# Optimization experiments

Measured on AMD Instinct MI355X. Metric: run time of the kernel, lower is better.

## Reference

```python
import jax, jax.numpy as jnp
import numpy as np

EMBED_DIM = 1024
N_HEADS = 16

def setup_inputs() -> dict:
    key = jax.random.key(0)
    ks = jax.random.split(key, 5)
    C = EMBED_DIM
    std = 1.0 / np.sqrt(C)
    x = jax.random.normal(ks[0], (2, 2048, C), dtype=jnp.float32)
    w_attn = jax.random.normal(ks[1], (C, 3 * C), dtype=jnp.float32) * std  # (in, out)
    b_attn = jax.random.normal(ks[2], (3 * C,), dtype=jnp.float32) * 0.01
    w_proj = jax.random.normal(ks[3], (C, C), dtype=jnp.float32) * std
    b_proj = jax.random.normal(ks[4], (C,), dtype=jnp.float32) * 0.01
    return {"x": x, "w_attn": w_attn, "b_attn": b_attn, "w_proj": w_proj, "b_proj": b_proj}

def reference(x, w_attn, b_attn, w_proj, b_proj):
    B, T, C = x.shape
    H = N_HEADS
    D = C // H
    qkv = x @ w_attn + b_attn                      # (B, T, 3C)
    q, k, v = jnp.split(qkv, 3, axis=2)
    # (B, T, C) -> (B, H, T, D)
    q = q.reshape(B, T, H, D).transpose(0, 2, 1, 3)
    k = k.reshape(B, T, H, D).transpose(0, 2, 1, 3)
    v = v.reshape(B, T, H, D).transpose(0, 2, 1, 3)
    # Faithful to source: query is divided by scale BEFORE QK^T, and the
    # similarity is divided by scale AGAIN before softmax (net scale = 1/D).
    scale = jnp.asarray(D, dtype=x.dtype) ** 0.5
    q = q / scale
    sim = jnp.einsum('bhnd,bhsd->bhns', q, k)      # (B, H, T, T)
    causal = jnp.tril(jnp.ones((T, T), dtype=bool))
    neg_min = jnp.finfo(sim.dtype).min
    sim = jnp.where(causal[None, None, :, :], sim, neg_min)
    attn = jax.nn.softmax(sim / scale, axis=-1)
    out = jnp.einsum('bhns,bhsd->bhnd', attn, v)   # (B, H, T, D)
    # source: gqa returns (b n h d), forward does transpose(1,2) -> (b h n d)
    # then .view(B, T, C); net effect is reshaping the (B,H,T,D) layout.
    y = out.reshape(B, T, C)
    y = y @ w_proj + b_proj
    return y
```

## Files before the change

kernel.cpp:

```cpp
#include <hip/hip_runtime.h>
#include <hip/hip_bf16.h>

#define BB 2
#define TT 2048
#define CC 1024
#define HH 16
#define DD 64
#define MM (BB*TT)
#define QSZ ((size_t)MM*CC)

#define QSCALE 0.022542110013890053f

typedef __attribute__((ext_vector_type(8))) short bf16x8;
typedef __attribute__((ext_vector_type(4))) float f32x4;
typedef __attribute__((address_space(1))) const unsigned char as1_u8;
typedef __attribute__((address_space(3))) unsigned char as3_u8;

struct alignas(8) bf16x4_s { __hip_bfloat16 h[4]; };

static __device__ __forceinline__ unsigned cvt_pk_bf16(float lo, float hi) {
    unsigned r;
    asm("v_cvt_pk_bf16_f32 %0, %1, %2" : "=v"(r) : "v"(lo), "v"(hi));
    return r;
}

static __device__ __forceinline__ float fast_exp2(float x) {
    return __builtin_amdgcn_exp2f(x);
}

__constant__ unsigned char U_qi[60] = {
    11,22,23,23, 10,20,21,21,22,30,31,31,
    9,18,19,19,20,27,28,28,29,29,29,30,30,31,
    8,16,17,17,18,24,25,25,26,26,26,27,27,28,
    7,14,15,15,16,24,24,25,
    6,12,13,13,14,
    5,12, 4,3,2,1,0};
__constant__ unsigned char U_t0[60] = {
    0,0,0,12, 0,0,0,11,12,0,0,11,
    0,0,0,10,11,0,0,10,0,10,20,11,21,22,
    0,0,0,9,10,0,0,9,0,9,18,10,19,20,
    0,0,0,8,9,9,17,18,
    0,0,0,7,8,
    0,7, 0,0,0,0,0};
__constant__ unsigned char U_t1[60] = {
    12,12,12,24, 11,11,11,22,23,11,11,22,
    10,10,10,20,21,10,10,20,10,20,30,21,31,32,
    9,9,9,18,19,9,9,18,9,18,27,19,28,29,
    8,8,8,16,17,17,25,26,
    7,7,7,14,15,
    6,13, 5,4,3,2,1};
__constant__ unsigned char U_pu[60] = {
    255,20,22,23, 255,16,18,19,21,42,45,46,
    255,12,14,15,17,33,36,37,39,40,41,43,44,47,
    255,8,10,11,13,24,27,28,30,31,32,34,35,38,
    255,4,6,7,9,25,26,29,
    255,0,2,3,5,
    255,1, 255,255,255,255,255};

__global__ __launch_bounds__(256) void prep_kernel(
    const float* __restrict__ x,  __hip_bfloat16* __restrict__ xb,
    const float* __restrict__ wa, __hip_bfloat16* __restrict__ wqkvT,
    const float* __restrict__ wp, __hip_bfloat16* __restrict__ wprojT)
{
    __shared__ float tile[64][68];
    const int t = threadIdx.x;
    const int b = blockIdx.x;
    if (b < 2048) {
        const int i = (b * 256 + t) * 8;
        const float4 a = *(const float4*)&x[i];
        const float4 c = *(const float4*)&x[i + 4];
        uint2 lo, hi;
        lo.x = cvt_pk_bf16(a.x, a.y); lo.y = cvt_pk_bf16(a.z, a.w);
        hi.x = cvt_pk_bf16(c.x, c.y); hi.y = cvt_pk_bf16(c.z, c.w);
        *(uint2*)&xb[i] = lo;
        *(uint2*)&xb[i + 4] = hi;
        return;
    }
    const float* in; __hip_bfloat16* outp; int R, Cc, bx, by;
    if (b < 2816) { const int i = b - 2048; in = wa; outp = wqkvT; R = CC; Cc = 3*CC; bx = i % 48; by = i / 48; }
    else          { const int i = b - 2816; in = wp; outp = wprojT; R = CC; Cc = CC;  bx = i % 16; by = i / 16; }
    const int c0 = bx * 64, r0 = by * 64;
    {
        const int r = t >> 2, cb = (t & 3) * 16;
        #pragma unroll
        for (int i = 0; i < 4; ++i)
            *(float4*)&tile[r][cb + i*4] = *(const float4*)&in[(size_t)(r0 + r)*Cc + c0 + cb + i*4];
    }
    __syncthreads();
    {
        const int c = t >> 2, rb = (t & 3) * 16;
        uint2 o0, o1;
        o0.x = cvt_pk_bf16(tile[rb+0][c],  tile[rb+1][c]);
        o0.y = cvt_pk_bf16(tile[rb+2][c],  tile[rb+3][c]);
        o1.x = cvt_pk_bf16(tile[rb+4][c],  tile[rb+5][c]);
        o1.y = cvt_pk_bf16(tile[rb+6][c],  tile[rb+7][c]);
        __hip_bfloat16* dst = outp + (size_t)(c0 + c)*R + r0 + rb;
        *(uint2*)&dst[0] = o0; *(uint2*)&dst[4] = o1;
        o0.x = cvt_pk_bf16(tile[rb+8][c],  tile[rb+9][c]);
        o0.y = cvt_pk_bf16(tile[rb+10][c], tile[rb+11][c]);
        o1.x = cvt_pk_bf16(tile[rb+12][c], tile[rb+13][c]);
        o1.y = cvt_pk_bf16(tile[rb+14][c], tile[rb+15][c]);
        *(uint2*)&dst[8] = o0; *(uint2*)&dst[12] = o1;
    }
}

template<int MODE>
__global__ __launch_bounds__(256) void gemm_mfma(
    const __hip_bfloat16* __restrict__ A,
    const __hip_bfloat16* __restrict__ BT,
    const float* __restrict__ bias,
    void* __restrict__ out, int M, int N, int K)
{
    __shared__ __hip_bfloat16 As[128][64];
    __shared__ __hip_bfloat16 Bs[128][64];

    const int tid = threadIdx.x;
    const int w = tid >> 6, l = tid & 63;
    const int lr = l & 15, lg = l >> 4;
    const int wr = w >> 1, wc = w & 1;
    const int rsw = (lr & 7) << 4;
    const int lsw = ((l & 7) ^ (l >> 3)) * 8;

    const int nwg = gridDim.x * gridDim.y;
    const int bid = blockIdx.y * gridDim.x + blockIdx.x;
    const int swz_id = (bid & 7) * (nwg >> 3) + (bid >> 3);
    const int row0 = (swz_id / gridDim.x) * 128;
    const int col0 = (swz_id % gridDim.x) * 128;

    f32x4 acc[4][4] = {};

    for (int k0 = 0; k0 < K; k0 += 64) {
        __syncthreads();
        #pragma unroll
        for (int i = 0; i < 4; ++i) {
            const int br = w*32 + i*8;
            const __hip_bfloat16* ga = A  + (size_t)(row0 + br + (l>>3))*K + k0 + lsw;
            __builtin_amdgcn_global_load_lds((as1_u8*)ga, (as3_u8*)&As[br][0], 16, 0, 0);
            const __hip_bfloat16* gb = BT + (size_t)(col0 + br + (l>>3))*K + k0 + lsw;
            __builtin_amdgcn_global_load_lds((as1_u8*)gb, (as3_u8*)&Bs[br][0], 16, 0, 0);
        }
        __syncthreads();

        #pragma unroll
        for (int s = 0; s < 2; ++s) {
            bf16x8 af[4], bfr[4];
            #pragma unroll
            for (int m = 0; m < 4; ++m) {
                const char* ab = (const char*)&As[wr*64 + m*16 + lr][0];
                af[m] = *(const bf16x8*)(ab + ((s*64 + lg*16) ^ rsw));
            }
            #pragma unroll
            for (int n = 0; n < 4; ++n) {
                const char* bb = (const char*)&Bs[wc*64 + n*16 + lr][0];
                bfr[n] = *(const bf16x8*)(bb + ((s*64 + lg*16) ^ rsw));
            }
            #pragma unroll
            for (int m = 0; m < 4; ++m)
                #pragma unroll
                for (int n = 0; n < 4; ++n)
                    acc[m][n] = __builtin_amdgcn_mfma_f32_16x16x32_bf16(af[m], bfr[n], acc[m][n], 0, 0, 0);
        }
    }

    #pragma unroll
    for (int m = 0; m < 4; ++m) {
        #pragma unroll
        for (int n = 0; n < 4; ++n) {
            const int ng = col0 + wc*64 + n*16 + lr;
            const float bv = bias[ng];
            const int mg0 = row0 + wr*64 + m*16 + lg*4;
            if (MODE == 0) {
                const int which = ng >> 10, c = ng & 1023;
                const int h = c >> 6, d = c & 63;
                if (which == 2) {
                    const int b = mg0 >> 11, t0 = mg0 & 2047;
                    uint2 pv;
                    pv.x = cvt_pk_bf16(acc[m][n][0] + bv, acc[m][n][1] + bv);
                    pv.y = cvt_pk_bf16(acc[m][n][2] + bv, acc[m][n][3] + bv);
                    *(uint2*)((__hip_bfloat16*)out + (size_t)2*QSZ +
                        (((size_t)(b*HH + h))*DD + d)*TT + t0) = pv;
                } else {
                    #pragma unroll
                    for (int r = 0; r < 4; ++r) {
                        const int mg = mg0 + r;
                        float v = acc[m][n][r] + bv;
                        if (which == 0) v *= QSCALE;
                        const int b = mg >> 11, t = mg & 2047;
                        ((__hip_bfloat16*)out)[(size_t)which*QSZ +
                            (((size_t)(b*HH + h))*TT + t)*DD + d] = __float2bfloat16(v);
                    }
                }
            } else {
                #pragma unroll
                for (int r = 0; r < 4; ++r)
                    ((float*)out)[(size_t)(mg0 + r)*N + ng] = acc[m][n][r] + bv;
            }
        }
    }
}

__global__ __launch_bounds__(256) void attn_mfma(
    const __hip_bfloat16* __restrict__ Qb,
    const __hip_bfloat16* __restrict__ Kb,
    const __hip_bfloat16* __restrict__ Vb,
    __hip_bfloat16* __restrict__ Ob,
    __hip_bfloat16* __restrict__ Opart,
    float* __restrict__ Lpart)
{
    __shared__ __hip_bfloat16 k_lds[64][64];
    __shared__ __hip_bfloat16 vT[64][64];
    __shared__ __hip_bfloat16 p_lds[4][16][64];

    const int tid = threadIdx.x;
    const int w  = tid >> 6;
    const int l  = tid & 63;
    const int lr = l & 15;
    const int lg = l >> 4;
    const int swz = (lr & 7) << 4;

    const int bid  = blockIdx.x;
    const int loc  = bid >> 3;
    const int bh   = (bid & 7) * 4 + (loc & 3);
    const int u    = loc >> 2;
    const int qi   = U_qi[u];
    const int t0i  = U_t0[u];
    const int t1i  = U_t1[u];
    const int pu   = U_pu[u];
    const int qb   = qi * 64;

    const __hip_bfloat16* Qh = Qb + (size_t)bh*TT*DD;
    const __hip_bfloat16* Kh = Kb + (size_t)bh*TT*DD;
    const __hip_bfloat16* Vh = Vb + (size_t)bh*DD*TT;

    bf16x8 qa[2];
    const int qrow = qb + w*16 + lr;
    {
        const __hip_bfloat16* qp = Qh + (size_t)qrow*DD + lg*8;
        qa[0] = *(const bf16x8*)(qp);
        qa[1] = *(const bf16x8*)(qp + 32);
    }

    const int off0 = (16*lg) ^ swz;
    const int off1 = (64 + 16*lg) ^ swz;
    const char* kr0b = (const char*)&k_lds[lr][0];
    const char* vr0b = (const char*)&vT[lr][0];
    char* pwb = (char*)&p_lds[w][lr][0];
    int pwo[4];
    #pragma unroll
    for (int mt = 0; mt < 4; ++mt) pwo[mt] = (32*mt + 8*lg) ^ swz;

    const int srow = tid >> 2, sch = tid & 3;
    const int wswz = (srow & 7) << 4;
    char* kwr = (char*)&k_lds[srow][0];
    char* vwr = (char*)&vT[srow][0];
    const int wo0 = (sch*32) ^ wswz, wo1 = (sch*32 + 16) ^ wswz;

    const __hip_bfloat16* ksrc = Kh + (size_t)(t0i*64 + srow)*DD + sch*16;
    const __hip_bfloat16* vsrc = Vh + (size_t)srow*TT + t0i*64 + sch*16;

    float4 kr0 = *(const float4*)ksrc, kr1 = *(const float4*)(ksrc + 8);
    float4 vr0 = *(const float4*)vsrc, vr1 = *(const float4*)(vsrc + 8);
    ksrc += 64*DD; vsrc += 64;
    *(float4*)(kwr + wo0) = kr0; *(float4*)(kwr + wo1) = kr1;
    *(float4*)(vwr + wo0) = vr0; *(float4*)(vwr + wo1) = vr1;
    __syncthreads();

    f32x4 oacc[4] = {};
    f32x4 lacc = {0.f, 0.f, 0.f, 0.f};

    for (int t = t0i; t < t1i; ++t) {
        const int kv0 = t * 64;
        const bool has_next = (t + 1 < t1i);

        if (has_next) {
            kr0 = *(const float4*)ksrc; kr1 = *(const float4*)(ksrc + 8);
            vr0 = *(const float4*)vsrc; vr1 = *(const float4*)(vsrc + 8);
            ksrc += 64*DD; vsrc += 64;
        }

        f32x4 sacc[4] = {};
        __builtin_amdgcn_s_setprio(1);
        #pragma unroll
        for (int mt = 0; mt < 4; ++mt) {
            const bf16x8 kb0 = *(const bf16x8*)(kr0b + mt*2048 + off0);
            const bf16x8 kb1 = *(const bf16x8*)(kr0b + mt*2048 + off1);
            sacc[mt] = __builtin_amdgcn_mfma_f32_16x16x32_bf16(kb0, qa[0], sacc[mt], 0, 0, 0);
            sacc[mt] = __builtin_amdgcn_mfma_f32_16x16x32_bf16(kb1, qa[1], sacc[mt], 0, 0, 0);
        }
        __builtin_amdgcn_s_setprio(0);

        if (t == qi) {
            #pragma unroll
            for (int mt = 0; mt < 4; ++mt)
                #pragma unroll
                for (int r = 0; r < 4; ++r)
                    if (kv0 + mt*16 + lg*4 + r > qrow) sacc[mt][r] = -3.0e38f;
        }
        #pragma unroll
        for (int mt = 0; mt < 4; ++mt) {
            const float p0 = fast_exp2(sacc[mt][0]), p1 = fast_exp2(sacc[mt][1]);
            const float p2 = fast_exp2(sacc[mt][2]), p3 = fast_exp2(sacc[mt][3]);
            lacc[mt] += (p0 + p1) + (p2 + p3);
            uint2 pp;
            pp.x = cvt_pk_bf16(p0, p1);
            pp.y = cvt_pk_bf16(p2, p3);
            *(uint2*)(pwb + pwo[mt]) = pp;
        }

        const bf16x8 pb0 = *(const bf16x8*)(pwb + off0);
        const bf16x8 pb1 = *(const bf16x8*)(pwb + off1);
        __builtin_amdgcn_s_setprio(1);
        #pragma unroll
        for (int dt = 0; dt < 4; ++dt) {
            const bf16x8 vb0 = *(const bf16x8*)(vr0b + dt*2048 + off0);
            const bf16x8 vb1 = *(const bf16x8*)(vr0b + dt*2048 + off1);
            oacc[dt] = __builtin_amdgcn_mfma_f32_16x16x32_bf16(vb0, pb0, oacc[dt], 0, 0, 0);
            oacc[dt] = __builtin_amdgcn_mfma_f32_16x16x32_bf16(vb1, pb1, oacc[dt], 0, 0, 0);
        }
        __builtin_amdgcn_s_setprio(0);

        if (has_next) {
            __syncthreads();
            *(float4*)(kwr + wo0) = kr0; *(float4*)(kwr + wo1) = kr1;
            *(float4*)(vwr + wo0) = vr0; *(float4*)(vwr + wo1) = vr1;
            __syncthreads();
        }
    }

    float l_r = (lacc[0] + lacc[1]) + (lacc[2] + lacc[3]);
    l_r += __shfl_xor(l_r, 16);
    l_r += __shfl_xor(l_r, 32);

    if (pu != 255) {
        const int unit = bh*48 + pu;
        const int rowu = w*16 + lr;
        __hip_bfloat16* Oprow = Opart + ((size_t)unit*64 + rowu)*64;
        #pragma unroll
        for (int dt = 0; dt < 4; ++dt) {
            uint2 ov;
            ov.x = cvt_pk_bf16(oacc[dt][0], oacc[dt][1]);
            ov.y = cvt_pk_bf16(oacc[dt][2], oacc[dt][3]);
            *(uint2*)(Oprow + dt*16 + lg*4) = ov;
        }
        if (lg == 0) Lpart[unit*64 + rowu] = l_r;
    } else {
        __hip_bfloat16* Orow = Ob + ((size_t)bh*TT + qrow)*DD;
        const float inv = 1.0f / l_r;
        #pragma unroll
        for (int dt = 0; dt < 4; ++dt) {
            uint2 ov;
            ov.x = cvt_pk_bf16(oacc[dt][0]*inv, oacc[dt][1]*inv);
            ov.y = cvt_pk_bf16(oacc[dt][2]*inv, oacc[dt][3]*inv);
            *(uint2*)(Orow + dt*16 + lg*4) = ov;
        }
    }
}

__global__ __launch_bounds__(256) void attn_combine(
    const __hip_bfloat16* __restrict__ Opart,
    const float* __restrict__ Lpart,
    __hip_bfloat16* __restrict__ Ob)
{
    const int w = threadIdx.x >> 6, d = threadIdx.x & 63;
    const int rowg = blockIdx.x * 4 + w;
    const int bh  = rowg / 1280;
    const int rem = rowg - bh * 1280;
    const int spb = rem >> 6;
    const int r   = rem & 63;
    const int nu  = (spb < 12) ? 2 : 3;
    const int pu0 = bh*48 + ((spb < 12) ? 2*spb : 24 + 3*(spb - 12));
    float o = 0.f, lsum = 0.f;
    for (int i = 0; i < nu; ++i) {
        o    += __bfloat162float(Opart[((size_t)(pu0 + i)*64 + r)*64 + d]);
        lsum += Lpart[(pu0 + i)*64 + r];
    }
    const int qrow = (12 + spb)*64 + r;
    Ob[((size_t)bh*TT + qrow)*DD + d] = __float2bfloat16(o / lsum);
}

extern "C" void kernel_launch(void* const* d_in, const int* in_sizes, int n_in,
                              void* d_out, int out_size, void* d_ws, size_t ws_size,
                              hipStream_t stream)
{
    const float* x      = (const float*)d_in[0];
    const float* w_attn = (const float*)d_in[1];
    const float* b_attn = (const float*)d_in[2];
    const float* w_proj = (const float*)d_in[3];
    const float* b_proj = (const float*)d_in[4];
    float* out = (float*)d_out;

    __hip_bfloat16* xb     = (__hip_bfloat16*)d_ws;
    __hip_bfloat16* wqkvT  = xb + QSZ;
    __hip_bfloat16* wprojT = wqkvT + 3*CC*CC;
    __hip_bfloat16* Qb     = wprojT + CC*CC;
    __hip_bfloat16* Kb     = Qb + QSZ;
    __hip_bfloat16* Vt     = Kb + QSZ;
    __hip_bfloat16* Ob     = Vt + QSZ;

    __hip_bfloat16* Opart  = xb;
    float*          Lpart  = (float*)(xb + (size_t)1536*64*64);

    prep_kernel<<<dim3(3072), 256, 0, stream>>>(x, xb, w_attn, wqkvT, w_proj, wprojT);

    gemm_mfma<0><<<dim3(3*CC/128, MM/128), 256, 0, stream>>>(xb, wqkvT, b_attn, (void*)Qb, MM, 3*CC, CC);

    attn_mfma<<<dim3(1920), 256, 0, stream>>>(Qb, Kb, Vt, Ob, Opart, Lpart);

    attn_combine<<<dim3(40960/4), 256, 0, stream>>>(Opart, Lpart, Ob);

    gemm_mfma<1><<<dim3(CC/128, MM/128), 256, 0, stream>>>(Ob, wprojT, b_proj, (void*)out, MM, CC, CC);
}
```

Before: 109.5 us.

## Double attention query tile to 128 rows with 512-thread blocks sharing K/V

Each attention block now covers 128 query rows with 8 waves instead of 64 rows with 4, so every K/V tile staged in LDS is reused by twice as many waves. The K and V loads are split across the two thread halves, halving per-thread global-load work. The work-split tables, partial-output indexing and combine kernel are rebuilt for 128-row units. Waves whose rows lie entirely above the diagonal of a tile skip its compute. The trade-off is fewer blocks, coarser causal load balance, and idle waves on diagonal tiles.

```diff
diff --git a/kernel.cpp b/kernel.cpp
--- a/kernel.cpp
+++ b/kernel.cpp
@@ -28,34 +28,18 @@
     return __builtin_amdgcn_exp2f(x);
 }
 
-__constant__ unsigned char U_qi[60] = {
-    11,22,23,23, 10,20,21,21,22,30,31,31,
-    9,18,19,19,20,27,28,28,29,29,29,30,30,31,
-    8,16,17,17,18,24,25,25,26,26,26,27,27,28,
-    7,14,15,15,16,24,24,25,
-    6,12,13,13,14,
-    5,12, 4,3,2,1,0};
-__constant__ unsigned char U_t0[60] = {
-    0,0,0,12, 0,0,0,11,12,0,0,11,
-    0,0,0,10,11,0,0,10,0,10,20,11,21,22,
-    0,0,0,9,10,0,0,9,0,9,18,10,19,20,
-    0,0,0,8,9,9,17,18,
-    0,0,0,7,8,
-    0,7, 0,0,0,0,0};
-__constant__ unsigned char U_t1[60] = {
-    12,12,12,24, 11,11,11,22,23,11,11,22,
-    10,10,10,20,21,10,10,20,10,20,30,21,31,32,
-    9,9,9,18,19,9,9,18,9,18,27,19,28,29,
-    8,8,8,16,17,17,25,26,
-    7,7,7,14,15,
-    6,13, 5,4,3,2,1};
-__constant__ unsigned char U_pu[60] = {
-    255,20,22,23, 255,16,18,19,21,42,45,46,
-    255,12,14,15,17,33,36,37,39,40,41,43,44,47,
-    255,8,10,11,13,24,27,28,30,31,32,34,35,38,
-    255,4,6,7,9,25,26,29,
-    255,0,2,3,5,
-    255,1, 255,255,255,255,255};
+__constant__ unsigned char U_sqi[30] = {
+    5,11,11,10,10,15,15, 4,9,9,13,14,14,14,15, 8,8,12,12,13,13,
+    3,7,7,12, 6,6, 2,1,0};
+__constant__ unsigned char U_t0[30] = {
+    0,0,12,0,11,0,11, 0,0,10,0,0,10,20,22, 0,9,0,9,10,19,
+    0,0,8,18, 0,7, 0,0,0};
+__constant__ unsigned char U_t1[30] = {
+    12,12,24,11,22,11,22, 10,10,20,10,10,20,30,32, 9,18,9,18,19,28,
+    8,8,16,26, 7,14, 6,4,2};
+__constant__ unsigned char U_pu[30] = {
+    255,10,11,8,9,21,22, 255,6,7,15,18,19,20,23, 4,5,12,13,16,17,
+    255,2,3,14, 0,1, 255,255,255};
 
 __global__ __launch_bounds__(256) void prep_kernel(
     const float* __restrict__ x,  __hip_bfloat16* __restrict__ xb,
@@ -199,7 +183,7 @@
     }
 }
 
-__global__ __launch_bounds__(256) void attn_mfma(
+__global__ __launch_bounds__(512) void attn_mfma(
     const __hip_bfloat16* __restrict__ Qb,
     const __hip_bfloat16* __restrict__ Kb,
     const __hip_bfloat16* __restrict__ Vb,
@@ -209,7 +193,7 @@
 {
     __shared__ __hip_bfloat16 k_lds[64][64];
     __shared__ __hip_bfloat16 vT[64][64];
-    __shared__ __hip_bfloat16 p_lds[4][16][64];
+    __shared__ __hip_bfloat16 p_lds[8][16][64];
 
     const int tid = threadIdx.x;
     const int w  = tid >> 6;
@@ -222,11 +206,11 @@
     const int loc  = bid >> 3;
     const int bh   = (bid & 7) * 4 + (loc & 3);
     const int u    = loc >> 2;
-    const int qi   = U_qi[u];
+    const int sqi  = U_sqi[u];
     const int t0i  = U_t0[u];
     const int t1i  = U_t1[u];
     const int pu   = U_pu[u];
-    const int qb   = qi * 64;
+    const int qb   = sqi * 128;
 
     const __hip_bfloat16* Qh = Qb + (size_t)bh*TT*DD;
     const __hip_bfloat16* Kh = Kb + (size_t)bh*TT*DD;
@@ -249,20 +233,20 @@
     #pragma unroll
     for (int mt = 0; mt < 4; ++mt) pwo[mt] = (32*mt + 8*lg) ^ swz;
 
-    const int srow = tid >> 2, sch = tid & 3;
+    const int sthalf = tid >> 8;
+    const int stid = tid & 255;
+    const int srow = stid >> 2, sch = stid & 3;
     const int wswz = (srow & 7) << 4;
-    char* kwr = (char*)&k_lds[srow][0];
-    char* vwr = (char*)&vT[srow][0];
+    char* swr = sthalf ? (char*)&vT[srow][0] : (char*)&k_lds[srow][0];
     const int wo0 = (sch*32) ^ wswz, wo1 = (sch*32 + 16) ^ wswz;
-
-    const __hip_bfloat16* ksrc = Kh + (size_t)(t0i*64 + srow)*DD + sch*16;
-    const __hip_bfloat16* vsrc = Vh + (size_t)srow*TT + t0i*64 + sch*16;
-
-    float4 kr0 = *(const float4*)ksrc, kr1 = *(const float4*)(ksrc + 8);
-    float4 vr0 = *(const float4*)vsrc, vr1 = *(const float4*)(vsrc + 8);
-    ksrc += 64*DD; vsrc += 64;
-    *(float4*)(kwr + wo0) = kr0; *(float4*)(kwr + wo1) = kr1;
-    *(float4*)(vwr + wo0) = vr0; *(float4*)(vwr + wo1) = vr1;
+    const __hip_bfloat16* ssrc = sthalf
+        ? (Vh + (size_t)srow*TT + t0i*64 + sch*16)
+        : (Kh + (size_t)(t0i*64 + srow)*DD + sch*16);
+    const size_t sstride = sthalf ? 64 : (size_t)64*DD;
+
+    float4 sr0 = *(const float4*)ssrc, sr1 = *(const float4*)(ssrc + 8);
+    ssrc += sstride;
+    *(float4*)(swr + wo0) = sr0; *(float4*)(swr + wo1) = sr1;
     __syncthreads();
 
     f32x4 oacc[4] = {};
@@ -273,56 +257,57 @@
         const bool has_next = (t + 1 < t1i);
 
         if (has_next) {
-            kr0 = *(const float4*)ksrc; kr1 = *(const float4*)(ksrc + 8);
-            vr0 = *(const float4*)vsrc; vr1 = *(const float4*)(vsrc + 8);
-            ksrc += 64*DD; vsrc += 64;
-        }
-
-        f32x4 sacc[4] = {};
-        __builtin_amdgcn_s_setprio(1);
-        #pragma unroll
-        for (int mt = 0; mt < 4; ++mt) {
-            const bf16x8 kb0 = *(const bf16x8*)(kr0b + mt*2048 + off0);
-            const bf16x8 kb1 = *(const bf16x8*)(kr0b + mt*2048 + off1);
-            sacc[mt] = __builtin_amdgcn_mfma_f32_16x16x32_bf16(kb0, qa[0], sacc[mt], 0, 0, 0);
-            sacc[mt] = __builtin_amdgcn_mfma_f32_16x16x32_bf16(kb1, qa[1], sacc[mt], 0, 0, 0);
-        }
-        __builtin_amdgcn_s_setprio(0);
-
-        if (t == qi) {
-            #pragma unroll
-            for (int mt = 0; mt < 4; ++mt)
+            sr0 = *(const float4*)ssrc; sr1 = *(const float4*)(ssrc + 8);
+            ssrc += sstride;
+        }
+
+        const bool dead = (w < 4) && (t == 2*sqi + 1);
+        if (!dead) {
+            f32x4 sacc[4] = {};
+            __builtin_amdgcn_s_setprio(1);
+            #pragma unroll
+            for (int mt = 0; mt < 4; ++mt) {
+                const bf16x8 kb0 = *(const bf16x8*)(kr0b + mt*2048 + off0);
+                const bf16x8 kb1 = *(const bf16x8*)(kr0b + mt*2048 + off1);
+                sacc[mt] = __builtin_amdgcn_mfma_f32_16x16x32_bf16(kb0, qa[0], sacc[mt], 0, 0, 0);
+                sacc[mt] = __builtin_amdgcn_mfma_f32_16x16x32_bf16(kb1, qa[1], sacc[mt], 0, 0, 0);
+            }
+            __builtin_amdgcn_s_setprio(0);
+
+            if (t >= 2*sqi) {
                 #pragma unroll
-                for (int r = 0; r < 4; ++r)
-                    if (kv0 + mt*16 + lg*4 + r > qrow) sacc[mt][r] = -3.0e38f;
-        }
-        #pragma unroll
-        for (int mt = 0; mt < 4; ++mt) {
-            const float p0 = fast_exp2(sacc[mt][0]), p1 = fast_exp2(sacc[mt][1]);
-            const float p2 = fast_exp2(sacc[mt][2]), p3 = fast_exp2(sacc[mt][3]);
-            lacc[mt] += (p0 + p1) + (p2 + p3);
-            uint2 pp;
-            pp.x = cvt_pk_bf16(p0, p1);
-            pp.y = cvt_pk_bf16(p2, p3);
-            *(uint2*)(pwb + pwo[mt]) = pp;
-        }
-
-        const bf16x8 pb0 = *(const bf16x8*)(pwb + off0);
-        const bf16x8 pb1 = *(const bf16x8*)(pwb + off1);
-        __builtin_amdgcn_s_setprio(1);
-        #pragma unroll
-        for (int dt = 0; dt < 4; ++dt) {
-            const bf16x8 vb0 = *(const bf16x8*)(vr0b + dt*2048 + off0);
-            const bf16x8 vb1 = *(const bf16x8*)(vr0b + dt*2048 + off1);
-            oacc[dt] = __builtin_amdgcn_mfma_f32_16x16x32_bf16(vb0, pb0, oacc[dt], 0, 0, 0);
-            oacc[dt] = __builtin_amdgcn_mfma_f32_16x16x32_bf16(vb1, pb1, oacc[dt], 0, 0, 0);
-        }
-        __builtin_amdgcn_s_setprio(0);
+                for (int mt = 0; mt < 4; ++mt)
+                    #pragma unroll
+                    for (int r = 0; r < 4; ++r)
+                        if (kv0 + mt*16 + lg*4 + r > qrow) sacc[mt][r] = -3.0e38f;
+            }
+            #pragma unroll
+            for (int mt = 0; mt < 4; ++mt) {
+                const float p0 = fast_exp2(sacc[mt][0]), p1 = fast_exp2(sacc[mt][1]);
+                const float p2 = fast_exp2(sacc[mt][2]), p3 = fast_exp2(sacc[mt][3]);
+                lacc[mt] += (p0 + p1) + (p2 + p3);
+                uint2 pp;
+                pp.x = cvt_pk_bf16(p0, p1);
+                pp.y = cvt_pk_bf16(p2, p3);
+                *(uint2*)(pwb + pwo[mt]) = pp;
+            }
+
+            const bf16x8 pb0 = *(const bf16x8*)(pwb + off0);
+            const bf16x8 pb1 = *(const bf16x8*)(pwb + off1);
+            __builtin_amdgcn_s_setprio(1);
+            #pragma unroll
+            for (int dt = 0; dt < 4; ++dt) {
+                const bf16x8 vb0 = *(const bf16x8*)(vr0b + dt*2048 + off0);
+                const bf16x8 vb1 = *(const bf16x8*)(vr0b + dt*2048 + off1);
+                oacc[dt] = __builtin_amdgcn_mfma_f32_16x16x32_bf16(vb0, pb0, oacc[dt], 0, 0, 0);
+                oacc[dt] = __builtin_amdgcn_mfma_f32_16x16x32_bf16(vb1, pb1, oacc[dt], 0, 0, 0);
+            }
+            __builtin_amdgcn_s_setprio(0);
+        }
 
         if (has_next) {
             __syncthreads();
-            *(float4*)(kwr + wo0) = kr0; *(float4*)(kwr + wo1) = kr1;
-            *(float4*)(vwr + wo0) = vr0; *(float4*)(vwr + wo1) = vr1;
+            *(float4*)(swr + wo0) = sr0; *(float4*)(swr + wo1) = sr1;
             __syncthreads();
         }
     }
@@ -332,9 +317,9 @@
     l_r += __shfl_xor(l_r, 32);
 
     if (pu != 255) {
-        const int unit = bh*48 + pu;
+        const int unit = bh*24 + pu;
         const int rowu = w*16 + lr;
-        __hip_bfloat16* Oprow = Opart + ((size_t)unit*64 + rowu)*64;
+        __hip_bfloat16* Oprow = Opart + ((size_t)unit*128 + rowu)*64;
         #pragma unroll
         for (int dt = 0; dt < 4; ++dt) {
             uint2 ov;
@@ -342,7 +327,7 @@
             ov.y = cvt_pk_bf16(oacc[dt][2], oacc[dt][3]);
             *(uint2*)(Oprow + dt*16 + lg*4) = ov;
         }
-        if (lg == 0) Lpart[unit*64 + rowu] = l_r;
+        if (lg == 0) Lpart[unit*128 + rowu] = l_r;
     } else {
         __hip_bfloat16* Orow = Ob + ((size_t)bh*TT + qrow)*DD;
         const float inv = 1.0f / l_r;
@@ -365,16 +350,16 @@
     const int rowg = blockIdx.x * 4 + w;
     const int bh  = rowg / 1280;
     const int rem = rowg - bh * 1280;
-    const int spb = rem >> 6;
-    const int r   = rem & 63;
-    const int nu  = (spb < 12) ? 2 : 3;
-    const int pu0 = bh*48 + ((spb < 12) ? 2*spb : 24 + 3*(spb - 12));
+    const int spb = rem >> 7;
+    const int r   = rem & 127;
+    const int nu  = (spb < 6) ? 2 : 3;
+    const int pu0 = bh*24 + ((spb < 6) ? 2*spb : 12 + 3*(spb - 6));
     float o = 0.f, lsum = 0.f;
     for (int i = 0; i < nu; ++i) {
-        o    += __bfloat162float(Opart[((size_t)(pu0 + i)*64 + r)*64 + d]);
-        lsum += Lpart[(pu0 + i)*64 + r];
-    }
-    const int qrow = (12 + spb)*64 + r;
+        o    += __bfloat162float(Opart[((size_t)(pu0 + i)*128 + r)*64 + d]);
+        lsum += Lpart[(pu0 + i)*128 + r];
+    }
+    const int qrow = (6 + spb)*128 + r;
     Ob[((size_t)bh*TT + qrow)*DD + d] = __float2bfloat16(o / lsum);
 }
 
@@ -398,13 +383,13 @@
     __hip_bfloat16* Ob     = Vt + QSZ;
 
     __hip_bfloat16* Opart  = xb;
-    float*          Lpart  = (float*)(xb + (size_t)1536*64*64);
+    float*          Lpart  = (float*)(xb + (size_t)768*128*64);
 
     prep_kernel<<<dim3(3072), 256, 0, stream>>>(x, xb, w_attn, wqkvT, w_proj, wprojT);
 
     gemm_mfma<0><<<dim3(3*CC/128, MM/128), 256, 0, stream>>>(xb, wqkvT, b_attn, (void*)Qb, MM, 3*CC, CC);
 
-    attn_mfma<<<dim3(1920), 256, 0, stream>>>(Qb, Kb, Vt, Ob, Opart, Lpart);
+    attn_mfma<<<dim3(960), 512, 0, stream>>>(Qb, Kb, Vt, Ob, Opart, Lpart);
 
     attn_combine<<<dim3(40960/4), 256, 0, stream>>>(Opart, Lpart, Ob);
 
```

New measurement: 105.6 us, median of 2. 1.04x faster.
